# Kernel optimization log

Hardware: AMD Instinct MI355X
Metric: run time of the kernel (lower is better)

The kernel has to match this reference:

```python
import jax, jax.numpy as jnp
import numpy as np

BQ = 64  # query block size
BK = 64  # key block size
PV_SCALE = 1e-3  # pvthreshd (~0..50) -> prob threshold, mirrors int8 P-quantization cutoff


def setup_inputs() -> dict:
    key = jax.random.key(0)
    ks = jax.random.split(key, 6)
    B, H, L, D = 2, 16, 2048, 64
    q = jax.random.normal(ks[0], (B, H, L, D), jnp.float32)
    k = jax.random.normal(ks[1], (B, H, L, D), jnp.float32)
    v = jax.random.normal(ks[2], (B, H, L, D), jnp.float32)
    # per-head tuned thresholds (init defaults / autotune ranges)
    cdfthreshd = 0.85 + 0.14 * jax.random.uniform(ks[3], (H,), jnp.float32)
    simthreshd1 = jax.random.uniform(ks[4], (H,), jnp.float32, minval=-0.3, maxval=0.5)
    pvthreshd = jax.random.uniform(ks[5], (H,), jnp.float32, minval=15.0, maxval=25.0)
    return dict(q=q, k=k, v=v, cdfthreshd=cdfthreshd,
                simthreshd1=simthreshd1, pvthreshd=pvthreshd)


def _sparse_meansim_attention(q, k, v, cdfthreshd, simthreshd1, pvthreshd):
    B, H, L, D = q.shape
    nqb, nkb = L // BQ, L // BK
    scale = 1.0 / jnp.sqrt(jnp.float32(D))

    # smooth_k: subtract per-(B,H) key mean along sequence
    k = k - k.mean(axis=2, keepdims=True)

    qb = q.reshape(B, H, nqb, BQ, D)
    kb = k.reshape(B, H, nkb, BK, D)
    qm = qb.mean(axis=3)  # [B,H,nqb,D]
    km = kb.mean(axis=3)  # [B,H,nkb,D]

    # mean cosine similarity of queries to their block mean -> pooled (prunable) blocks
    qn = jnp.linalg.norm(qb, axis=-1)            # [B,H,nqb,BQ]
    qmn = jnp.linalg.norm(qm, axis=-1)           # [B,H,nqb]
    cos = jnp.einsum('bhnqd,bhnd->bhnq', qb, qm) / (qn * qmn[..., None] + 1e-6)
    pooled = cos.mean(axis=-1) > simthreshd1[None, :, None]  # [B,H,nqb]

    # block-level score map from pooled means, CDF-based top-mass block selection
    s = jnp.einsum('bhid,bhjd->bhij', qm, km) * scale        # [B,H,nqb,nkb]
    p = jax.nn.softmax(s, axis=-1)
    order = jnp.argsort(-p, axis=-1)
    p_sorted = jnp.take_along_axis(p, order, axis=-1)
    excl_cdf = jnp.cumsum(p_sorted, axis=-1) - p_sorted      # exclusive CDF
    keep_sorted = excl_cdf < cdfthreshd[None, :, None, None]
    keep = jnp.take_along_axis(keep_sorted, jnp.argsort(order, axis=-1), axis=-1)

    sink = (jnp.arange(nkb) == 0)  # attention_sink: always keep first key block
    block_mask = keep | (~pooled)[..., None] | sink          # [B,H,nqb,nkb]

    # full attention restricted to selected blocks
    S = jnp.einsum('bhqd,bhkd->bhqk', q, k) * scale          # [B,H,L,L]
    m = jnp.repeat(jnp.repeat(block_mask, BQ, axis=2), BK, axis=3)
    P = jax.nn.softmax(jnp.where(m, S, -jnp.inf), axis=-1)

    # second-stage PV pruning: skip PV accumulation for negligible prob blocks
    Pb = P.reshape(B, H, nqb, BQ, nkb, BK)
    pv_keep = Pb.max(axis=(3, 5)) >= pvthreshd[None, :, None, None] * PV_SCALE
    pv_keep = pv_keep | sink
    Pb = Pb * pv_keep[:, :, :, None, :, None].astype(P.dtype)

    o = jnp.einsum('bhqk,bhkd->bhqd', Pb.reshape(B, H, L, L), v)
    return o


def reference(q, k, v, cdfthreshd, simthreshd1, pvthreshd):
    return _sparse_meansim_attention(q, k, v, cdfthreshd, simthreshd1, pvthreshd)
```

## Files before the change

kernel.cpp:

```cpp
#include <hip/hip_runtime.h>
#include <math.h>
#include <stdint.h>

#define B 2
#define H 16
#define L 2048
#define D 64
#define NB 32
#define PTS 72

typedef unsigned short u16;
typedef unsigned int u32;
typedef __attribute__((ext_vector_type(4))) unsigned short u16x4;
typedef __attribute__((ext_vector_type(8))) unsigned short u16x8;
typedef __attribute__((ext_vector_type(8))) short s16x8;
typedef __attribute__((ext_vector_type(4))) float f32x4;

__device__ __forceinline__ void bf16split(float f, u16& hi, u16& lo) {
  union { float f; uint32_t u; } a; a.f = f;
  uint32_t r = (a.u + 0x7fffu + ((a.u >> 16) & 1u)) >> 16;
  hi = (u16)r;
  union { uint32_t u; float f; } b; b.u = r << 16;
  float res = f - b.f;
  union { float f; uint32_t u; } c; c.f = res;
  uint32_t r2 = (c.u + 0x7fffu + ((c.u >> 16) & 1u)) >> 16;
  lo = (u16)r2;
}

__global__ __launch_bounds__(256) void k_prep(const float* __restrict__ k,
                                              const float* __restrict__ v,
                                              float* __restrict__ ksum,
                                              u16* __restrict__ khi_g,
                                              u16* __restrict__ klo_g,
                                              u16* __restrict__ vthi_g,
                                              u16* __restrict__ vtlo_g,
                                              float* __restrict__ kmax2g) {
  int blk = blockIdx.x, bh = blk >> 5, j = blk & 31, t = threadIdx.x;
  __shared__ float vt[64 * 65];
  __shared__ float pk_[4][64];
  __shared__ unsigned bmaxS;
  if (t == 0) bmaxS = 0u;
  size_t base = (size_t)blk * 4096;
  {
    int d = t & 63, g = t >> 6;
    float sk = 0.f;
    for (int r = g * 16; r < g * 16 + 16; ++r) sk += k[base + r * 64 + d];
    pk_[g][d] = sk;
  }
  __syncthreads();
  if (t < 64) ksum[(size_t)blk * 64 + t] = pk_[0][t] + pk_[1][t] + pk_[2][t] + pk_[3][t];

  float rmax = 0.f;
  for (int it = 0; it < 4; ++it) {
    int idx = t + 256 * it, r = idx >> 4, c4 = (idx & 15) * 4;
    float4 f = *(const float4*)(k + base + r * 64 + c4);
    u16 h0,l0,h1,l1,h2,l2,h3,l3;
    bf16split(f.x,h0,l0); bf16split(f.y,h1,l1); bf16split(f.z,h2,l2); bf16split(f.w,h3,l3);
    *(u16x4*)(khi_g + base + r * 64 + c4) = (u16x4){h0,h1,h2,h3};
    *(u16x4*)(klo_g + base + r * 64 + c4) = (u16x4){l0,l1,l2,l3};
    float ssq = f.x*f.x + f.y*f.y + f.z*f.z + f.w*f.w;
    ssq += __shfl_xor(ssq, 1); ssq += __shfl_xor(ssq, 2);
    ssq += __shfl_xor(ssq, 4); ssq += __shfl_xor(ssq, 8);
    if ((t & 15) == 0) rmax = fmaxf(rmax, ssq);
    float4 g2 = *(const float4*)(v + base + r * 64 + c4);
    vt[(c4 + 0) * 65 + r] = g2.x;
    vt[(c4 + 1) * 65 + r] = g2.y;
    vt[(c4 + 2) * 65 + r] = g2.z;
    vt[(c4 + 3) * 65 + r] = g2.w;
  }
  if ((t & 15) == 0) atomicMax(&bmaxS, __float_as_uint(rmax));
  __syncthreads();
  if (t == 0) atomicMax((unsigned*)(kmax2g + bh), bmaxS);
  for (int it = 0; it < 2; ++it) {
    int idx = t + 256 * it, d = idx >> 3, s8 = (idx & 7) * 8;
    u16x8 vh8, vl8;
    for (int ii = 0; ii < 8; ++ii) {
      u16 hh, ll; bf16split(vt[d * 65 + s8 + ii], hh, ll);
      vh8[ii] = hh; vl8[ii] = ll;
    }
    size_t o = (size_t)bh * 131072 + (size_t)d * 2048 + j * 64 + s8;
    *(u16x8*)(vthi_g + o) = vh8;
    *(u16x8*)(vtlo_g + o) = vl8;
  }
}

__global__ __launch_bounds__(256, 3) void k_attn(
    const float* __restrict__ q,
    const float* __restrict__ ksum,
    const u16* __restrict__ khi_g, const u16* __restrict__ klo_g,
    const u16* __restrict__ vthi_g, const u16* __restrict__ vtlo_g,
    const float* __restrict__ cdfthreshd, const float* __restrict__ simthreshd1,
    const float* __restrict__ pvthreshd, const float* __restrict__ kmax2g,
    float* __restrict__ out) {
  int blk = blockIdx.x, bh = blk >> 5, i = blk & 31, h = bh & (H - 1);
  int t = threadIdx.x, lane = t & 63, w = t >> 6;
  int m16 = lane & 15, quad = lane >> 4;

  __shared__ __align__(16) uint8_t smem[47120];
  float* qf32  = (float*)smem;
  u32*   rbm   = (u32*)(smem + 36864);
  float* MS    = (float*)(smem + 45312);
  float* linvS = (float*)(smem + 45568);
  float* lpart = (float*)(smem + 45824);
  float* qmS   = (float*)(smem + 46848);
  int*   pooledS = (int*)(smem + 47104);
  u32*   mwS     = (u32*)(smem + 47108);
  u32*   gmS     = (u32*)(smem + 47112);
#define PBUF(b, pl) ((u16*)(smem + ((b) * 2 + (pl)) * 9216))

  const float* qg = q + ((size_t)bh * L + (size_t)i * 64) * D;
  const u16* kh = khi_g + (size_t)bh * (L * D);
  const u16* kl = klo_g + (size_t)bh * (L * D);
  const u16* vh = vthi_g + (size_t)bh * (L * D);
  const u16* vl = vtlo_g + (size_t)bh * (L * D);

  s16x8 qhf[4][2], qlf[4][2];
#pragma unroll
  for (int nt = 0; nt < 4; ++nt)
#pragma unroll
    for (int ks = 0; ks < 2; ++ks) {
      const float* p0 = qg + (16 * nt + m16) * 64 + ks * 32 + quad * 8;
      float4 a = *(const float4*)p0;
      float4 b2 = *(const float4*)(p0 + 4);
      u16 hh[8], ll[8];
      bf16split(a.x,  hh[0], ll[0]); bf16split(a.y,  hh[1], ll[1]);
      bf16split(a.z,  hh[2], ll[2]); bf16split(a.w,  hh[3], ll[3]);
      bf16split(b2.x, hh[4], ll[4]); bf16split(b2.y, hh[5], ll[5]);
      bf16split(b2.z, hh[6], ll[6]); bf16split(b2.w, hh[7], ll[7]);
      qhf[nt][ks] = (s16x8){(short)hh[0],(short)hh[1],(short)hh[2],(short)hh[3],
                            (short)hh[4],(short)hh[5],(short)hh[6],(short)hh[7]};
      qlf[nt][ks] = (s16x8){(short)ll[0],(short)ll[1],(short)ll[2],(short)ll[3],
                            (short)ll[4],(short)ll[5],(short)ll[6],(short)ll[7]};
    }
  for (int it = 0; it < 4; ++it) {
    int idx = t + 256 * it, r = idx >> 4, c4 = (idx & 15) * 4;
    *(float4*)&qf32[r * 68 + c4] = ((const float4*)qg)[idx];
  }
  for (int e = t; e < 64 * 33; e += 256) rbm[e] = 0x7F800000u;
  __syncthreads();

  if (w == 0) {
    float s = 0.f;
    for (int r = 0; r < 64; ++r) s += qf32[r * 68 + lane];
    qmS[lane] = s * (1.f / 64.f);
  }
  __syncthreads();

  bool keepj = false;
  if (w == 0 && lane < 32) {
    int j = lane;
    const float* ksp = ksum + (size_t)bh * NB * 64 + j * 64;
    float sv = 0.f;
    for (int d = 0; d < 64; ++d) sv += qmS[d] * ksp[d];
    sv *= (1.f / 64.f) * 0.125f;
    float mx = sv;
    for (int off = 16; off; off >>= 1) mx = fmaxf(mx, __shfl_xor(mx, off, 32));
    float p = expf(sv - mx);
    float sum = p;
    for (int off = 16; off; off >>= 1) sum += __shfl_xor(sum, off, 32);
    p /= sum;
    float excl = 0.f;
    for (int u = 0; u < 32; ++u) {
      float pu = __shfl(p, u, 32);
      if ((pu > p) || (pu == p && u < j)) excl += pu;
    }
    keepj = excl < cdfthreshd[h];
  }
  if (w == 1) {
    int r = lane;
    float dot = 0.f, qn2 = 0.f, qmn2 = 0.f;
    for (int d = 0; d < 64; ++d) {
      float a = qf32[r * 68 + d], b2 = qmS[d];
      dot += a * b2; qn2 += a * a; qmn2 += b2 * b2;
    }
    float cs = dot / (sqrtf(qn2) * sqrtf(qmn2) + 1e-6f);
    float su = cs;
    for (int off = 32; off; off >>= 1) su += __shfl_xor(su, off);
    if (lane == 0) *pooledS = (su * (1.f / 64.f)) > simthreshd1[h];
    MS[r] = sqrtf(qn2 * kmax2g[bh]) * 0.125f;
  }
  __syncthreads();
  if (w == 0 && lane < 32) {
    bool bit = keepj || !(*pooledS) || (lane == 0);
    unsigned long long bal = __ballot(bit);
    if (lane == 0) *mwS = (u32)bal;
  }
  __syncthreads();
  u32 mw = *mwS;

  float Mq[4];
#pragma unroll
  for (int nt = 0; nt < 4; ++nt) Mq[nt] = MS[16 * nt + m16];

  float lp[4] = {0.f, 0.f, 0.f, 0.f};
  {
    int j = (int)__builtin_ctz(mw);
    u32 rm_ = mw & (mw - 1);
    s16x8 ka[2][2], kan[2][2];
    const u16* kr0 = kh + (size_t)(j * 64 + 16 * w + m16) * 64 + quad * 8;
    const u16* kl0 = kl + (size_t)(j * 64 + 16 * w + m16) * 64 + quad * 8;
#pragma unroll
    for (int ks = 0; ks < 2; ++ks) {
      ka[ks][0] = *(const s16x8*)(kr0 + ks * 32);
      ka[ks][1] = *(const s16x8*)(kl0 + ks * 32);
    }
    for (;;) {
      int nj = -1;
      if (rm_) {
        nj = (int)__builtin_ctz(rm_); rm_ &= rm_ - 1;
        const u16* nr = kh + (size_t)(nj * 64 + 16 * w + m16) * 64 + quad * 8;
        const u16* nl = kl + (size_t)(nj * 64 + 16 * w + m16) * 64 + quad * 8;
#pragma unroll
        for (int ks = 0; ks < 2; ++ks) {
          kan[ks][0] = *(const s16x8*)(nr + ks * 32);
          kan[ks][1] = *(const s16x8*)(nl + ks * 32);
        }
      }
      f32x4 acc[4];
#pragma unroll
      for (int nt = 0; nt < 4; ++nt) acc[nt] = (f32x4){0.f, 0.f, 0.f, 0.f};
#pragma unroll
      for (int ks = 0; ks < 2; ++ks)
#pragma unroll
        for (int nt = 0; nt < 4; ++nt) {
          acc[nt] = __builtin_amdgcn_mfma_f32_16x16x32_bf16(ka[ks][0], qhf[nt][ks], acc[nt], 0, 0, 0);
          acc[nt] = __builtin_amdgcn_mfma_f32_16x16x32_bf16(ka[ks][1], qhf[nt][ks], acc[nt], 0, 0, 0);
          acc[nt] = __builtin_amdgcn_mfma_f32_16x16x32_bf16(ka[ks][0], qlf[nt][ks], acc[nt], 0, 0, 0);
        }
#pragma unroll
      for (int nt = 0; nt < 4; ++nt) {
        float vmax = -1e30f;
#pragma unroll
        for (int reg = 0; reg < 4; ++reg) {
          float s = acc[nt][reg] * 0.125f - Mq[nt];
          lp[nt] += __expf(s);
          vmax = fmaxf(vmax, s);
        }
        vmax = fmaxf(vmax, __shfl_xor(vmax, 16));
        vmax = fmaxf(vmax, __shfl_xor(vmax, 32));
        if (quad == 0)
          atomicMin(&rbm[(16 * nt + m16) * 33 + j], __float_as_uint(fmaxf(-vmax, 0.f)));
      }
      if (nj < 0) break;
#pragma unroll
      for (int ks = 0; ks < 2; ++ks) { ka[ks][0] = kan[ks][0]; ka[ks][1] = kan[ks][1]; }
      j = nj;
    }
  }
#pragma unroll
  for (int nt = 0; nt < 4; ++nt) {
    float s = lp[nt];
    s += __shfl_xor(s, 16); s += __shfl_xor(s, 32);
    if (quad == 0) lpart[w * 64 + 16 * nt + m16] = s;
  }
  __syncthreads();
  if (t < 64) linvS[t] = 1.f / (lpart[t] + lpart[64 + t] + lpart[128 + t] + lpart[192 + t]);
  __syncthreads();

  if (t < 32) {
    bool keep = (mw >> t) & 1u;
    if (keep && t != 0) {
      float thr = pvthreshd[h] * 1e-3f;
      float mp = 0.f;
      for (int r = 0; r < 64; ++r) {
        float key = __uint_as_float(rbm[r * 33 + t]);
        mp = fmaxf(mp, __expf(-key) * linvS[r]);
      }
      keep = mp >= thr;
    }
    unsigned long long bal = __ballot(keep);
    if (t == 0) *gmS = (u32)bal;
  }
  __syncthreads();
  u32 gm = *gmS;

  float linq[4];
#pragma unroll
  for (int nt = 0; nt < 4; ++nt) linq[nt] = linvS[16 * nt + m16];
  f32x4 oacc[4];
#pragma unroll
  for (int nt = 0; nt < 4; ++nt) oacc[nt] = (f32x4){0.f, 0.f, 0.f, 0.f};

  {
    int buf = 0;
    int j = -1;
    u32 g2 = gm;
    s16x8 ka[2][2];
    if (g2) {
      j = (int)__builtin_ctz(g2); g2 &= g2 - 1;
      const u16* kr0 = kh + (size_t)(j * 64 + 16 * w + m16) * 64 + quad * 8;
      const u16* kl0 = kl + (size_t)(j * 64 + 16 * w + m16) * 64 + quad * 8;
#pragma unroll
      for (int ks = 0; ks < 2; ++ks) {
        ka[ks][0] = *(const s16x8*)(kr0 + ks * 32);
        ka[ks][1] = *(const s16x8*)(kl0 + ks * 32);
      }
    }
    while (j >= 0) {
      s16x8 va[2][2];
      const u16* vr0 = vh + (size_t)(16 * w + m16) * L + j * 64 + quad * 8;
      const u16* vl0 = vl + (size_t)(16 * w + m16) * L + j * 64 + quad * 8;
#pragma unroll
      for (int ks = 0; ks < 2; ++ks) {
        va[ks][0] = *(const s16x8*)(vr0 + ks * 32);
        va[ks][1] = *(const s16x8*)(vl0 + ks * 32);
      }
      f32x4 acc[4];
#pragma unroll
      for (int nt = 0; nt < 4; ++nt) acc[nt] = (f32x4){0.f, 0.f, 0.f, 0.f};
#pragma unroll
      for (int ks = 0; ks < 2; ++ks)
#pragma unroll
        for (int nt = 0; nt < 4; ++nt) {
          acc[nt] = __builtin_amdgcn_mfma_f32_16x16x32_bf16(ka[ks][0], qhf[nt][ks], acc[nt], 0, 0, 0);
          acc[nt] = __builtin_amdgcn_mfma_f32_16x16x32_bf16(ka[ks][1], qhf[nt][ks], acc[nt], 0, 0, 0);
          acc[nt] = __builtin_amdgcn_mfma_f32_16x16x32_bf16(ka[ks][0], qlf[nt][ks], acc[nt], 0, 0, 0);
        }
      int nj = -1;
      if (g2) {
        nj = (int)__builtin_ctz(g2); g2 &= g2 - 1;
        const u16* nr = kh + (size_t)(nj * 64 + 16 * w + m16) * 64 + quad * 8;
        const u16* nl = kl + (size_t)(nj * 64 + 16 * w + m16) * 64 + quad * 8;
#pragma unroll
        for (int ks = 0; ks < 2; ++ks) {
          ka[ks][0] = *(const s16x8*)(nr + ks * 32);
          ka[ks][1] = *(const s16x8*)(nl + ks * 32);
        }
      }
      u16* ph_ = PBUF(buf, 0);
      u16* pl_ = PBUF(buf, 1);
#pragma unroll
      for (int nt = 0; nt < 4; ++nt) {
        u16x4 ph4, pl4;
#pragma unroll
        for (int reg = 0; reg < 4; ++reg) {
          float p = __expf(acc[nt][reg] * 0.125f - Mq[nt]) * linq[nt];
          u16 hh, ll; bf16split(p, hh, ll);
          ph4[reg] = hh; pl4[reg] = ll;
        }
        int off = (16 * nt + m16) * PTS + 16 * w + 4 * quad;
        *(u16x4*)(ph_ + off) = ph4;
        *(u16x4*)(pl_ + off) = pl4;
      }
      __syncthreads();
#pragma unroll
      for (int ks = 0; ks < 2; ++ks)
#pragma unroll
        for (int nt = 0; nt < 4; ++nt) {
          s16x8 pbh = *(const s16x8*)(ph_ + (16 * nt + m16) * PTS + ks * 32 + quad * 8);
          s16x8 pbl = *(const s16x8*)(pl_ + (16 * nt + m16) * PTS + ks * 32 + quad * 8);
          oacc[nt] = __builtin_amdgcn_mfma_f32_16x16x32_bf16(va[ks][0], pbh, oacc[nt], 0, 0, 0);
          oacc[nt] = __builtin_amdgcn_mfma_f32_16x16x32_bf16(va[ks][1], pbh, oacc[nt], 0, 0, 0);
          oacc[nt] = __builtin_amdgcn_mfma_f32_16x16x32_bf16(va[ks][0], pbl, oacc[nt], 0, 0, 0);
        }
      buf ^= 1;
      j = nj;
    }
  }

  float* ob = out + ((size_t)bh * L + (size_t)i * 64) * D;
#pragma unroll
  for (int nt = 0; nt < 4; ++nt)
    *(f32x4*)(ob + (16 * nt + m16) * 64 + 16 * w + 4 * quad) = oacc[nt];
}

extern "C" void kernel_launch(void* const* d_in, const int* in_sizes, int n_in,
                              void* d_out, int out_size, void* d_ws, size_t ws_size,
                              hipStream_t stream) {
  (void)in_sizes; (void)n_in; (void)out_size; (void)ws_size;
  const float* q   = (const float*)d_in[0];
  const float* k   = (const float*)d_in[1];
  const float* v   = (const float*)d_in[2];
  const float* cdf = (const float*)d_in[3];
  const float* sim = (const float*)d_in[4];
  const float* pvt = (const float*)d_in[5];
  float* out = (float*)d_out;

  uint8_t* w8 = (uint8_t*)d_ws;
  float* ksum  = (float*)w8;
  float* kmax2 = (float*)(w8 + 262144);
  u16* khi_g  = (u16*)(w8 + 262400);
  u16* klo_g  = khi_g + (size_t)B * H * L * D;
  u16* vthi_g = klo_g + (size_t)B * H * L * D;
  u16* vtlo_g = vthi_g + (size_t)B * H * L * D;

  hipMemsetAsync(kmax2, 0, B * H * sizeof(float), stream);
  k_prep<<<B * H * NB, 256, 0, stream>>>(k, v, ksum, khi_g, klo_g, vthi_g, vtlo_g, kmax2);
  k_attn<<<B * H * NB, 256, 0, stream>>>(q, ksum, khi_g, klo_g, vthi_g, vtlo_g,
                                         cdf, sim, pvt, kmax2, out);
}
```

Baseline: 240.4 us.

## Use packed bf16 conversion, single P buffer, more occupancy, head-major block order

Replaces the manual bf16 hi/lo split with packed __float22bfloat162_rn conversions that store 32-bit words. The double-buffered P tile becomes a single buffer with an extra barrier before each write, which frees enough shared memory to raise the launch-bound occupancy hint from 3 to 4 blocks. It also reorders block indexing so consecutive blocks cover different heads rather than different query blocks of one head. The costs are an extra __syncthreads per key block and possibly worse L2 reuse of K and V across neighbouring blocks.

```diff
diff --git a/kernel.cpp b/kernel.cpp
--- a/kernel.cpp
+++ b/kernel.cpp
@@ -1,4 +1,5 @@
 #include <hip/hip_runtime.h>
+#include <hip/hip_bf16.h>
 #include <math.h>
 #include <stdint.h>
 
@@ -11,20 +12,29 @@
 
 typedef unsigned short u16;
 typedef unsigned int u32;
+typedef __attribute__((ext_vector_type(2))) unsigned int u32x2;
 typedef __attribute__((ext_vector_type(4))) unsigned short u16x4;
 typedef __attribute__((ext_vector_type(8))) unsigned short u16x8;
 typedef __attribute__((ext_vector_type(8))) short s16x8;
 typedef __attribute__((ext_vector_type(4))) float f32x4;
 
-__device__ __forceinline__ void bf16split(float f, u16& hi, u16& lo) {
-  union { float f; uint32_t u; } a; a.f = f;
-  uint32_t r = (a.u + 0x7fffu + ((a.u >> 16) & 1u)) >> 16;
-  hi = (u16)r;
-  union { uint32_t u; float f; } b; b.u = r << 16;
-  float res = f - b.f;
-  union { float f; uint32_t u; } c; c.f = res;
-  uint32_t r2 = (c.u + 0x7fffu + ((c.u >> 16) & 1u)) >> 16;
-  lo = (u16)r2;
+union FragU { s16x8 v; u32 u[4]; };
+
+__device__ __forceinline__ u32 pkbf(float a, float b) {
+  __hip_bfloat162 h = __float22bfloat162_rn(make_float2(a, b));
+  union { __hip_bfloat162 h; u32 u; } cv; cv.h = h; return cv.u;
+}
+__device__ __forceinline__ float bf2f(u32 u16bits) {
+  union { u32 u; float f; } c; c.u = u16bits << 16; return c.f;
+}
+__device__ __forceinline__ void split4(float4 p, u32x2& hi, u32x2& lo) {
+  u32 h01 = pkbf(p.x, p.y), h23 = pkbf(p.z, p.w);
+  float rx = p.x - bf2f(h01 & 0xffffu);
+  float ry = p.y - bf2f(h01 >> 16);
+  float rz = p.z - bf2f(h23 & 0xffffu);
+  float rw = p.w - bf2f(h23 >> 16);
+  hi = (u32x2){h01, h23};
+  lo = (u32x2){pkbf(rx, ry), pkbf(rz, rw)};
 }
 
 __global__ __launch_bounds__(256) void k_prep(const float* __restrict__ k,
@@ -54,10 +64,9 @@
   for (int it = 0; it < 4; ++it) {
     int idx = t + 256 * it, r = idx >> 4, c4 = (idx & 15) * 4;
     float4 f = *(const float4*)(k + base + r * 64 + c4);
-    u16 h0,l0,h1,l1,h2,l2,h3,l3;
-    bf16split(f.x,h0,l0); bf16split(f.y,h1,l1); bf16split(f.z,h2,l2); bf16split(f.w,h3,l3);
-    *(u16x4*)(khi_g + base + r * 64 + c4) = (u16x4){h0,h1,h2,h3};
-    *(u16x4*)(klo_g + base + r * 64 + c4) = (u16x4){l0,l1,l2,l3};
+    u32x2 hi, lo; split4(f, hi, lo);
+    *(u32x2*)(khi_g + base + r * 64 + c4) = hi;
+    *(u32x2*)(klo_g + base + r * 64 + c4) = lo;
     float ssq = f.x*f.x + f.y*f.y + f.z*f.z + f.w*f.w;
     ssq += __shfl_xor(ssq, 1); ssq += __shfl_xor(ssq, 2);
     ssq += __shfl_xor(ssq, 4); ssq += __shfl_xor(ssq, 8);
@@ -73,18 +82,18 @@
   if (t == 0) atomicMax((unsigned*)(kmax2g + bh), bmaxS);
   for (int it = 0; it < 2; ++it) {
     int idx = t + 256 * it, d = idx >> 3, s8 = (idx & 7) * 8;
-    u16x8 vh8, vl8;
-    for (int ii = 0; ii < 8; ++ii) {
-      u16 hh, ll; bf16split(vt[d * 65 + s8 + ii], hh, ll);
-      vh8[ii] = hh; vl8[ii] = ll;
-    }
+    const float* vr = &vt[d * 65 + s8];
+    float4 f0 = {vr[0], vr[1], vr[2], vr[3]};
+    float4 f1 = {vr[4], vr[5], vr[6], vr[7]};
+    u32x2 h0, l0, h1, l1;
+    split4(f0, h0, l0); split4(f1, h1, l1);
     size_t o = (size_t)bh * 131072 + (size_t)d * 2048 + j * 64 + s8;
-    *(u16x8*)(vthi_g + o) = vh8;
-    *(u16x8*)(vtlo_g + o) = vl8;
-  }
-}
-
-__global__ __launch_bounds__(256, 3) void k_attn(
+    *(u32x2*)(vthi_g + o) = h0; *(u32x2*)(vthi_g + o + 4) = h1;
+    *(u32x2*)(vtlo_g + o) = l0; *(u32x2*)(vtlo_g + o + 4) = l1;
+  }
+}
+
+__global__ __launch_bounds__(256, 4) void k_attn(
     const float* __restrict__ q,
     const float* __restrict__ ksum,
     const u16* __restrict__ khi_g, const u16* __restrict__ klo_g,
@@ -92,21 +101,22 @@
     const float* __restrict__ cdfthreshd, const float* __restrict__ simthreshd1,
     const float* __restrict__ pvthreshd, const float* __restrict__ kmax2g,
     float* __restrict__ out) {
-  int blk = blockIdx.x, bh = blk >> 5, i = blk & 31, h = bh & (H - 1);
+  int blk = blockIdx.x, bh = blk & 31, i = blk >> 5, h = bh & (H - 1);
   int t = threadIdx.x, lane = t & 63, w = t >> 6;
   int m16 = lane & 15, quad = lane >> 4;
 
-  __shared__ __align__(16) uint8_t smem[47120];
+  __shared__ __align__(16) uint8_t smem[28688];
   float* qf32  = (float*)smem;
-  u32*   rbm   = (u32*)(smem + 36864);
-  float* MS    = (float*)(smem + 45312);
-  float* linvS = (float*)(smem + 45568);
-  float* lpart = (float*)(smem + 45824);
-  float* qmS   = (float*)(smem + 46848);
-  int*   pooledS = (int*)(smem + 47104);
-  u32*   mwS     = (u32*)(smem + 47108);
-  u32*   gmS     = (u32*)(smem + 47112);
-#define PBUF(b, pl) ((u16*)(smem + ((b) * 2 + (pl)) * 9216))
+  u32*   rbm   = (u32*)(smem + 18432);
+  float* MS    = (float*)(smem + 26880);
+  float* linvS = (float*)(smem + 27136);
+  float* lpart = (float*)(smem + 27392);
+  float* qmS   = (float*)(smem + 28416);
+  int*   pooledS = (int*)(smem + 28672);
+  u32*   mwS     = (u32*)(smem + 28676);
+  u32*   gmS     = (u32*)(smem + 28680);
+  u16* ph_ = (u16*)smem;
+  u16* pl_ = (u16*)(smem + 9216);
 
   const float* qg = q + ((size_t)bh * L + (size_t)i * 64) * D;
   const u16* kh = khi_g + (size_t)bh * (L * D);
@@ -122,15 +132,12 @@
       const float* p0 = qg + (16 * nt + m16) * 64 + ks * 32 + quad * 8;
       float4 a = *(const float4*)p0;
       float4 b2 = *(const float4*)(p0 + 4);
-      u16 hh[8], ll[8];
-      bf16split(a.x,  hh[0], ll[0]); bf16split(a.y,  hh[1], ll[1]);
-      bf16split(a.z,  hh[2], ll[2]); bf16split(a.w,  hh[3], ll[3]);
-      bf16split(b2.x, hh[4], ll[4]); bf16split(b2.y, hh[5], ll[5]);
-      bf16split(b2.z, hh[6], ll[6]); bf16split(b2.w, hh[7], ll[7]);
-      qhf[nt][ks] = (s16x8){(short)hh[0],(short)hh[1],(short)hh[2],(short)hh[3],
-                            (short)hh[4],(short)hh[5],(short)hh[6],(short)hh[7]};
-      qlf[nt][ks] = (s16x8){(short)ll[0],(short)ll[1],(short)ll[2],(short)ll[3],
-                            (short)ll[4],(short)ll[5],(short)ll[6],(short)ll[7]};
+      u32x2 ha, la, hb, lb;
+      split4(a, ha, la); split4(b2, hb, lb);
+      FragU fh, fl;
+      fh.u[0] = ha[0]; fh.u[1] = ha[1]; fh.u[2] = hb[0]; fh.u[3] = hb[1];
+      fl.u[0] = la[0]; fl.u[1] = la[1]; fl.u[2] = lb[0]; fl.u[3] = lb[1];
+      qhf[nt][ks] = fh.v; qlf[nt][ks] = fl.v;
     }
   for (int it = 0; it < 4; ++it) {
     int idx = t + 256 * it, r = idx >> 4, c4 = (idx & 15) * 4;
@@ -282,7 +289,6 @@
   for (int nt = 0; nt < 4; ++nt) oacc[nt] = (f32x4){0.f, 0.f, 0.f, 0.f};
 
   {
-    int buf = 0;
     int j = -1;
     u32 g2 = gm;
     s16x8 ka[2][2];
@@ -327,20 +333,18 @@
           ka[ks][1] = *(const s16x8*)(nl + ks * 32);
         }
       }
-      u16* ph_ = PBUF(buf, 0);
-      u16* pl_ = PBUF(buf, 1);
+      __syncthreads();
 #pragma unroll
       for (int nt = 0; nt < 4; ++nt) {
-        u16x4 ph4, pl4;
-#pragma unroll
-        for (int reg = 0; reg < 4; ++reg) {
-          float p = __expf(acc[nt][reg] * 0.125f - Mq[nt]) * linq[nt];
-          u16 hh, ll; bf16split(p, hh, ll);
-          ph4[reg] = hh; pl4[reg] = ll;
-        }
+        float4 pv;
+        pv.x = __expf(acc[nt][0] * 0.125f - Mq[nt]) * linq[nt];
+        pv.y = __expf(acc[nt][1] * 0.125f - Mq[nt]) * linq[nt];
+        pv.z = __expf(acc[nt][2] * 0.125f - Mq[nt]) * linq[nt];
+        pv.w = __expf(acc[nt][3] * 0.125f - Mq[nt]) * linq[nt];
+        u32x2 hi, lo; split4(pv, hi, lo);
         int off = (16 * nt + m16) * PTS + 16 * w + 4 * quad;
-        *(u16x4*)(ph_ + off) = ph4;
-        *(u16x4*)(pl_ + off) = pl4;
+        *(u32x2*)(ph_ + off) = hi;
+        *(u32x2*)(pl_ + off) = lo;
       }
       __syncthreads();
 #pragma unroll
@@ -353,7 +357,6 @@
           oacc[nt] = __builtin_amdgcn_mfma_f32_16x16x32_bf16(va[ks][1], pbh, oacc[nt], 0, 0, 0);
           oacc[nt] = __builtin_amdgcn_mfma_f32_16x16x32_bf16(va[ks][0], pbl, oacc[nt], 0, 0, 0);
         }
-      buf ^= 1;
       j = nj;
     }
   }
```

After: 339.4 us. 41.2% more time.
